# Performance work log

Hardware: AMD Instinct MI355X
Metric: run time of the kernel (lower is better)

The kernel has to match this reference:

```python
import math
import jax, jax.numpy as jnp
import numpy as np

B, T_ALL, D = 128, 197, 768
T = T_ALL - 1
ORG, E, DFF, NCLS = 5, 8, 1024, 100
CAP_FACTOR = 1.25
MAX_K = 2  # training=True -> min(2, n_experts)


def setup_inputs() -> dict:
    key = jax.random.key(0)
    ks = jax.random.split(key, 16)
    s = lambda *sh: 0.02
    inp = {
        "tokens": jax.random.normal(ks[0], (B, T_ALL, D), jnp.float32),
        "organ_priors": jax.random.uniform(ks[1], (B, ORG), jnp.float32),
        "router_w": jax.random.normal(ks[2], (D + ORG, E), jnp.float32) * 0.02,
        "router_b": jnp.zeros((E,), jnp.float32),
        "w1": jax.random.normal(ks[3], (E, D, DFF), jnp.float32) * 0.02,
        "b1": jnp.zeros((E, DFF), jnp.float32),
        "w2": jax.random.normal(ks[4], (E, DFF, D), jnp.float32) * 0.02,
        "b2": jnp.zeros((E, D), jnp.float32),
        "ln_g": jnp.ones((D,), jnp.float32),
        "ln_b": jnp.zeros((D,), jnp.float32),
        "cls_w": jax.random.normal(ks[5], (D, NCLS), jnp.float32) * 0.02,
        "cls_b": jnp.zeros((NCLS,), jnp.float32),
        "aux_w": jax.random.normal(ks[6], (D, ORG), jnp.float32) * 0.02,
        "aux_b": jnp.zeros((ORG,), jnp.float32),
    }
    return inp


def switch_moe(flat, flat_prior, router_w, router_b, w1, b1, w2, b2):
    N = flat.shape[0]
    capacity = math.ceil(N / E * CAP_FACTOR)  # static
    logits = jnp.concatenate([flat, flat_prior], axis=-1) @ router_w + router_b  # (N,E)
    probs = jax.nn.softmax(logits, axis=-1)
    entropy = -(probs * jnp.log(probs + 1e-12)).sum(-1)  # (N,)
    topk_vals, topk_idx = jax.lax.top_k(probs, MAX_K)  # (N,K)
    topk_probs = topk_vals / (topk_vals.sum(-1, keepdims=True) + 1e-12)
    # one-hot expert assignment over top-k slots: (N,E)
    sel = jnp.any(topk_idx[:, None, :] == jnp.arange(E)[None, :, None], axis=-1)
    # combine weight per (token, expert): first (unique) matching top-k slot's prob
    w_full = (topk_probs[:, None, :] * (topk_idx[:, None, :] == jnp.arange(E)[None, :, None])).sum(-1)  # (N,E)
    # capacity-limited dispatch: per expert keep top-`capacity` tokens by router prob
    score = jnp.where(sel, probs, -jnp.inf).T  # (E,N)
    top_scores, idx = jax.lax.top_k(score, capacity)  # (E,cap), sorted desc like torch.sort
    valid = jnp.isfinite(top_scores)  # (E,cap)
    gathered = flat[idx]  # (E,cap,D)
    h = jax.nn.gelu(jnp.einsum('ecd,edf->ecf', gathered, w1) + b1[:, None, :], approximate=False)
    out_sel = jnp.einsum('ecf,efd->ecd', h, w2) + b2[:, None, :]  # (E,cap,D)
    w_sel = jnp.take_along_axis(w_full.T, idx, axis=1) * valid  # (E,cap)
    flat_idx = idx.reshape(-1)
    outputs = jnp.zeros_like(flat).at[flat_idx].add((out_sel * w_sel[..., None]).reshape(-1, D))
    processed = jnp.zeros((N,), jnp.float32).at[flat_idx].add(valid.reshape(-1).astype(jnp.float32)) > 0
    outputs = jnp.where(processed[:, None], outputs, flat)
    return outputs, probs, entropy


def reference(tokens, organ_priors, router_w, router_b, w1, b1, w2, b2,
              ln_g, ln_b, cls_w, cls_b, aux_w, aux_b):
    cls = tokens[:, 0, :]                # (B,D)
    patches = tokens[:, 1:, :]           # (B,T,D)
    flat = patches.reshape(B * T, D)
    flat_prior = jnp.broadcast_to(organ_priors[:, None, :], (B, T, ORG)).reshape(B * T, ORG)
    out_flat, probs, entropy = switch_moe(flat, flat_prior, router_w, router_b, w1, b1, w2, b2)
    # cls token passes through MoE untouched (only patches go through switch)
    mu = cls.mean(-1, keepdims=True)
    var = ((cls - mu) ** 2).mean(-1, keepdims=True)
    cls_final = (cls - mu) * jax.lax.rsqrt(var + 1e-5) * ln_g + ln_b
    logits = cls_final @ cls_w + cls_b
    aux_org = cls_final @ aux_w + aux_b
    return logits, aux_org, probs.reshape(B, T, E), entropy.reshape(B, T)
```

## Files before the change

kernel.cpp:

```cpp
#include <hip/hip_runtime.h>
#include <hip/hip_bf16.h>
#include <math.h>

#define NB     128
#define NT_ALL 197
#define NT     196
#define ND     768
#define NORG   5
#define NE     8
#define NCLS   100
#define NCOL   105
#define NTOK   (NB * NT)
#define KB     24
#define PF     6

#define CBLKS  256
#define RBLKS  392

typedef short  bf16x8 __attribute__((ext_vector_type(8)));
typedef float  f32x4  __attribute__((ext_vector_type(4)));


__global__ __launch_bounds__(256, 4) void fused_kernel(
    const float* __restrict__ tokens,
    const float* __restrict__ priors,
    const float* __restrict__ rw,
    const float* __restrict__ rbias,
    const float* __restrict__ ln_g, const float* __restrict__ ln_b,
    const float* __restrict__ cls_w,
    const float* __restrict__ cls_b,
    const float* __restrict__ aux_w,
    const float* __restrict__ aux_b,
    float* __restrict__ out_logits,
    float* __restrict__ out_aux,
    float* __restrict__ probs_out,
    float* __restrict__ ent_out)
{
    const int t = threadIdx.x;

    if (blockIdx.x >= CBLKS) {
        const int rblk = blockIdx.x - CBLKS;

        __shared__ __align__(16) __hip_bfloat16 s_a[KB * 4 * 16 * 8];
        __shared__ float s_pl[2][NE];

        const int wid  = t >> 6;
        const int lane = t & 63;
        const int tok0 = rblk * 64;
        const int gbase = tok0 + wid * 16;
        const int tt = lane & 15;
        const int g  = lane >> 4;
        const int token = gbase + tt;
        const int b  = token / NT;
        const float* xp = tokens + ((size_t)b * NT_ALL + 1 + (token - b * NT)) * ND
                          + g * 8;

        float4 xb[PF][2];
#pragma unroll
        for (int i = 0; i < PF; ++i) {
            xb[i][0] = *reinterpret_cast<const float4*>(xp + i * 32);
            xb[i][1] = *reinterpret_cast<const float4*>(xp + i * 32 + 4);
        }

        {
            bf16x8 z = {0, 0, 0, 0, 0, 0, 0, 0};
            bf16x8* p = (bf16x8*)s_a;
            for (int i = t; i < KB * 4 * 8; i += 256)
                p[(i >> 3) * 16 + 8 + (i & 7)] = z;
        }
        for (int i = t; i < ND * NE; i += 256) {
            const int k = i >> 3, e = i & 7;
            const int kb = k >> 5, gg = (k >> 3) & 3, j = k & 7;
            s_a[(((kb * 4 + gg) * 16) + e) * 8 + j] = __float2bfloat16(rw[i]);
        }
        const int b0 = tok0 / NT;
        const int b1 = (tok0 + 63) / NT;
        if (t < 16) {
            const int e = t & 7, which = t >> 3;
            const int bb = which ? b1 : b0;
            float a = rbias[e];
#pragma unroll
            for (int o = 0; o < NORG; ++o)
                a = fmaf(priors[bb * NORG + o], rw[(ND + o) * NE + e], a);
            s_pl[which][e] = a;
        }
        __syncthreads();

        const bf16x8* s_a8 = (const bf16x8*)s_a;
        f32x4 acc0 = {0.f, 0.f, 0.f, 0.f};
        f32x4 acc1 = {0.f, 0.f, 0.f, 0.f};

#pragma unroll
        for (int kb = 0; kb < KB; ++kb) {
            const float4 x0 = xb[kb % PF][0];
            const float4 x1 = xb[kb % PF][1];
            union { bf16x8 v; __hip_bfloat16 h[8]; } u;
            u.h[0] = __float2bfloat16(x0.x);
            u.h[1] = __float2bfloat16(x0.y);
            u.h[2] = __float2bfloat16(x0.z);
            u.h[3] = __float2bfloat16(x0.w);
            u.h[4] = __float2bfloat16(x1.x);
            u.h[5] = __float2bfloat16(x1.y);
            u.h[6] = __float2bfloat16(x1.z);
            u.h[7] = __float2bfloat16(x1.w);
            const bf16x8 af = s_a8[(kb * 4 + g) * 16 + tt];
            if (kb & 1)
                acc1 = __builtin_amdgcn_mfma_f32_16x16x32_bf16(af, u.v, acc1, 0, 0, 0);
            else
                acc0 = __builtin_amdgcn_mfma_f32_16x16x32_bf16(af, u.v, acc0, 0, 0, 0);
            if (kb + PF < KB) {
                xb[kb % PF][0] = *reinterpret_cast<const float4*>(xp + (kb + PF) * 32);
                xb[kb % PF][1] = *reinterpret_cast<const float4*>(xp + (kb + PF) * 32 + 4);
            }
        }
        const f32x4 acc = acc0 + acc1;

        const float p0 = __shfl_xor(acc[0], 16, 64);
        const float p1 = __shfl_xor(acc[1], 16, 64);
        const float p2 = __shfl_xor(acc[2], 16, 64);
        const float p3 = __shfl_xor(acc[3], 16, 64);

        if (lane < 16) {
            float lg[NE] = {acc[0], acc[1], acc[2], acc[3], p0, p1, p2, p3};
            const int bsel = (token >= (b0 + 1) * NT) ? 1 : 0;
#pragma unroll
            for (int e = 0; e < NE; ++e) lg[e] += s_pl[bsel][e];

            float m = lg[0];
#pragma unroll
            for (int e = 1; e < NE; ++e) m = fmaxf(m, lg[e]);
            float S = 0.f, dd = 0.f;
#pragma unroll
            for (int e = 0; e < NE; ++e) {
                const float l = lg[e] - m;
                const float p = __expf(l);
                lg[e] = p;
                S += p;
                dd = fmaf(p, l, dd);
            }
            const float inv = 1.f / S;
            const float ent = __logf(S) - dd * inv;

            float4 q0 = {lg[0] * inv, lg[1] * inv, lg[2] * inv, lg[3] * inv};
            float4 q1 = {lg[4] * inv, lg[5] * inv, lg[6] * inv, lg[7] * inv};
            *reinterpret_cast<float4*>(probs_out + (size_t)token * NE)     = q0;
            *reinterpret_cast<float4*>(probs_out + (size_t)token * NE + 4) = q1;
            ent_out[token] = ent;
        }
    } else {
        const int cb   = blockIdx.x;
        const int b    = cb >> 1;
        const int half = cb & 1;
        const int lane = t & 63;
        const int wv   = t >> 6;

        __shared__ __align__(16) float s_x[ND];
        __shared__ float s_red[4];
        __shared__ float s_part[4][65];

        const float* xp = tokens + (size_t)b * NT_ALL * ND;

        float sum = 0.f;
        for (int i = t; i < ND; i += 256) { float v = xp[i]; s_x[i] = v; sum += v; }
#pragma unroll
        for (int off = 32; off; off >>= 1) sum += __shfl_xor(sum, off, 64);
        if (lane == 0) s_red[wv] = sum;
        __syncthreads();
        const float mu = (s_red[0] + s_red[1] + s_red[2] + s_red[3]) * (1.f / ND);
        __syncthreads();

        float sq = 0.f;
        for (int i = t; i < ND; i += 256) { float d = s_x[i] - mu; sq += d * d; }
#pragma unroll
        for (int off = 32; off; off >>= 1) sq += __shfl_xor(sq, off, 64);
        if (lane == 0) s_red[wv] = sq;
        __syncthreads();
        const float var  = (s_red[0] + s_red[1] + s_red[2] + s_red[3]) * (1.f / ND);
        const float rstd = rsqrtf(var + 1e-5f);
        __syncthreads();

        for (int i = t; i < ND; i += 256)
            s_x[i] = (s_x[i] - mu) * rstd * ln_g[i] + ln_b[i];
        __syncthreads();

        const int c = half * 64 + lane;
        const float* wp; int st;
        if (c < NCLS)      { wp = cls_w + c;          st = NCLS; }
        else if (c < NCOL) { wp = aux_w + (c - NCLS); st = NORG; }
        else               { wp = aux_w;              st = NORG; }

        const int d0 = wv * 192;
        const float* w = wp + (size_t)d0 * st;
        const int st2 = 2 * st, st3 = 3 * st, st4 = 4 * st;
        float a0 = 0.f, a1 = 0.f, a2 = 0.f, a3 = 0.f;
#pragma unroll 8
        for (int j = 0; j < 192; j += 4) {
            const float4 x4 = *reinterpret_cast<const float4*>(&s_x[d0 + j]);
            a0 = fmaf(x4.x, w[0],   a0);
            a1 = fmaf(x4.y, w[st],  a1);
            a2 = fmaf(x4.z, w[st2], a2);
            a3 = fmaf(x4.w, w[st3], a3);
            w += st4;
        }
        s_part[wv][lane] = (a0 + a1) + (a2 + a3);
        __syncthreads();

        if (t < 64) {
            float r = s_part[0][t] + s_part[1][t] + s_part[2][t] + s_part[3][t];
            const int cc = half * 64 + t;
            if (cc < NCLS)
                out_logits[b * NCLS + cc] = r + cls_b[cc];
            else if (cc < NCOL)
                out_aux[b * NORG + (cc - NCLS)] = r + aux_b[cc - NCLS];
        }
    }
}

extern "C" void kernel_launch(void* const* d_in, const int* in_sizes, int n_in,
                              void* d_out, int out_size, void* d_ws, size_t ws_size,
                              hipStream_t stream) {
    const float* tokens = (const float*)d_in[0];
    const float* priors = (const float*)d_in[1];
    const float* rw     = (const float*)d_in[2];
    const float* rbias  = (const float*)d_in[3];
    const float* ln_g   = (const float*)d_in[8];
    const float* ln_b   = (const float*)d_in[9];
    const float* cls_w  = (const float*)d_in[10];
    const float* cls_b  = (const float*)d_in[11];
    const float* aux_w  = (const float*)d_in[12];
    const float* aux_b  = (const float*)d_in[13];

    float* out = (float*)d_out;
    float* out_logits = out;
    float* out_aux    = out + NB * NCLS;
    float* out_probs  = out + NB * NCLS + NB * NORG;
    float* out_ent    = out + NB * NCLS + NB * NORG + (size_t)NTOK * NE;

    fused_kernel<<<CBLKS + RBLKS, 256, 0, stream>>>(
        tokens, priors, rw, rbias, ln_g, ln_b, cls_w, cls_b, aux_w, aux_b,
        out_logits, out_aux, out_probs, out_ent);
}
```

Baseline: 25.96 us.

## Precompute bf16 router weight fragments in a prepass and read them from global memory

A separate prepass kernel converts the router weights into MFMA-ready bf16 fragments and computes the per-batch prior+bias logit offsets, writing both to workspace. Each router block then skips its per-block LDS staging, conversion and __syncthreads, and instead loads the A fragments directly from global (L2-cached), prefetched one step ahead. Router blocks are also moved to the front of the grid ahead of the classifier blocks. The cost is an extra kernel launch and a dependency between the two kernels.

```diff
diff --git a/kernel.cpp b/kernel.cpp
--- a/kernel.cpp
+++ b/kernel.cpp
@@ -14,18 +14,54 @@
 #define KB     24
 #define PF     6
 
+#define RBLKS  392
 #define CBLKS  256
-#define RBLKS  392
+
+#define NFRAG  (KB * 64)
+#define WS_A_BYTES  (NFRAG * 16)
+#define WS_PL_OFF   WS_A_BYTES
 
 typedef short  bf16x8 __attribute__((ext_vector_type(8)));
 typedef float  f32x4  __attribute__((ext_vector_type(4)));
 
 
+__global__ __launch_bounds__(256) void prepass_kernel(
+    const float* __restrict__ rw,
+    const float* __restrict__ rbias,
+    const float* __restrict__ priors,
+    __hip_bfloat16* __restrict__ ws_a,
+    float* __restrict__ ws_pl)
+{
+    const int gi = blockIdx.x * 256 + threadIdx.x;
+    if (gi < NFRAG) {
+        const int e  = gi & 15;
+        const int kg = gi >> 4;
+        union { bf16x8 v; __hip_bfloat16 h[8]; } u;
+        if (e < 8) {
+#pragma unroll
+            for (int j = 0; j < 8; ++j)
+                u.h[j] = __float2bfloat16(rw[(kg * 8 + j) * NE + e]);
+        } else {
+#pragma unroll
+            for (int j = 0; j < 8; ++j)
+                u.h[j] = __float2bfloat16(0.f);
+        }
+        reinterpret_cast<bf16x8*>(ws_a)[gi] = u.v;
+    } else if (gi < NFRAG + NB * NE) {
+        const int i = gi - NFRAG;
+        const int b = i >> 3, e = i & 7;
+        float a = rbias[e];
+#pragma unroll
+        for (int o = 0; o < NORG; ++o)
+            a = fmaf(priors[b * NORG + o], rw[(ND + o) * NE + e], a);
+        ws_pl[i] = a;
+    }
+}
+
 __global__ __launch_bounds__(256, 4) void fused_kernel(
     const float* __restrict__ tokens,
-    const float* __restrict__ priors,
-    const float* __restrict__ rw,
-    const float* __restrict__ rbias,
+    const __hip_bfloat16* __restrict__ ws_a,
+    const float* __restrict__ ws_pl,
     const float* __restrict__ ln_g, const float* __restrict__ ln_b,
     const float* __restrict__ cls_w,
     const float* __restrict__ cls_b,
@@ -38,22 +74,16 @@
 {
     const int t = threadIdx.x;
 
-    if (blockIdx.x >= CBLKS) {
-        const int rblk = blockIdx.x - CBLKS;
-
-        __shared__ __align__(16) __hip_bfloat16 s_a[KB * 4 * 16 * 8];
-        __shared__ float s_pl[2][NE];
-
+    if (blockIdx.x < RBLKS) {
         const int wid  = t >> 6;
         const int lane = t & 63;
-        const int tok0 = rblk * 64;
-        const int gbase = tok0 + wid * 16;
-        const int tt = lane & 15;
-        const int g  = lane >> 4;
-        const int token = gbase + tt;
+        const int tt   = lane & 15;
+        const int g    = lane >> 4;
+        const int token = (blockIdx.x * 4 + wid) * 16 + tt;
         const int b  = token / NT;
         const float* xp = tokens + ((size_t)b * NT_ALL + 1 + (token - b * NT)) * ND
                           + g * 8;
+        const bf16x8* afp = reinterpret_cast<const bf16x8*>(ws_a) + lane;
 
         float4 xb[PF][2];
 #pragma unroll
@@ -61,37 +91,14 @@
             xb[i][0] = *reinterpret_cast<const float4*>(xp + i * 32);
             xb[i][1] = *reinterpret_cast<const float4*>(xp + i * 32 + 4);
         }
-
-        {
-            bf16x8 z = {0, 0, 0, 0, 0, 0, 0, 0};
-            bf16x8* p = (bf16x8*)s_a;
-            for (int i = t; i < KB * 4 * 8; i += 256)
-                p[(i >> 3) * 16 + 8 + (i & 7)] = z;
-        }
-        for (int i = t; i < ND * NE; i += 256) {
-            const int k = i >> 3, e = i & 7;
-            const int kb = k >> 5, gg = (k >> 3) & 3, j = k & 7;
-            s_a[(((kb * 4 + gg) * 16) + e) * 8 + j] = __float2bfloat16(rw[i]);
-        }
-        const int b0 = tok0 / NT;
-        const int b1 = (tok0 + 63) / NT;
-        if (t < 16) {
-            const int e = t & 7, which = t >> 3;
-            const int bb = which ? b1 : b0;
-            float a = rbias[e];
-#pragma unroll
-            for (int o = 0; o < NORG; ++o)
-                a = fmaf(priors[bb * NORG + o], rw[(ND + o) * NE + e], a);
-            s_pl[which][e] = a;
-        }
-        __syncthreads();
-
-        const bf16x8* s_a8 = (const bf16x8*)s_a;
+        bf16x8 af_cur = afp[0];
+
         f32x4 acc0 = {0.f, 0.f, 0.f, 0.f};
         f32x4 acc1 = {0.f, 0.f, 0.f, 0.f};
 
 #pragma unroll
         for (int kb = 0; kb < KB; ++kb) {
+            const bf16x8 af_next = (kb + 1 < KB) ? afp[(kb + 1) * 64] : af_cur;
             const float4 x0 = xb[kb % PF][0];
             const float4 x1 = xb[kb % PF][1];
             union { bf16x8 v; __hip_bfloat16 h[8]; } u;
@@ -103,15 +110,15 @@
             u.h[5] = __float2bfloat16(x1.y);
             u.h[6] = __float2bfloat16(x1.z);
             u.h[7] = __float2bfloat16(x1.w);
-            const bf16x8 af = s_a8[(kb * 4 + g) * 16 + tt];
             if (kb & 1)
-                acc1 = __builtin_amdgcn_mfma_f32_16x16x32_bf16(af, u.v, acc1, 0, 0, 0);
+                acc1 = __builtin_amdgcn_mfma_f32_16x16x32_bf16(af_cur, u.v, acc1, 0, 0, 0);
             else
-                acc0 = __builtin_amdgcn_mfma_f32_16x16x32_bf16(af, u.v, acc0, 0, 0, 0);
+                acc0 = __builtin_amdgcn_mfma_f32_16x16x32_bf16(af_cur, u.v, acc0, 0, 0, 0);
             if (kb + PF < KB) {
                 xb[kb % PF][0] = *reinterpret_cast<const float4*>(xp + (kb + PF) * 32);
                 xb[kb % PF][1] = *reinterpret_cast<const float4*>(xp + (kb + PF) * 32 + 4);
             }
+            af_cur = af_next;
         }
         const f32x4 acc = acc0 + acc1;
 
@@ -122,9 +129,10 @@
 
         if (lane < 16) {
             float lg[NE] = {acc[0], acc[1], acc[2], acc[3], p0, p1, p2, p3};
-            const int bsel = (token >= (b0 + 1) * NT) ? 1 : 0;
-#pragma unroll
-            for (int e = 0; e < NE; ++e) lg[e] += s_pl[bsel][e];
+            const float4 pl0 = *reinterpret_cast<const float4*>(ws_pl + b * NE);
+            const float4 pl1 = *reinterpret_cast<const float4*>(ws_pl + b * NE + 4);
+            lg[0] += pl0.x; lg[1] += pl0.y; lg[2] += pl0.z; lg[3] += pl0.w;
+            lg[4] += pl1.x; lg[5] += pl1.y; lg[6] += pl1.z; lg[7] += pl1.w;
 
             float m = lg[0];
 #pragma unroll
@@ -148,7 +156,7 @@
             ent_out[token] = ent;
         }
     } else {
-        const int cb   = blockIdx.x;
+        const int cb   = blockIdx.x - RBLKS;
         const int b    = cb >> 1;
         const int half = cb & 1;
         const int lane = t & 63;
@@ -236,7 +244,14 @@
     float* out_probs  = out + NB * NCLS + NB * NORG;
     float* out_ent    = out + NB * NCLS + NB * NORG + (size_t)NTOK * NE;
 
-    fused_kernel<<<CBLKS + RBLKS, 256, 0, stream>>>(
-        tokens, priors, rw, rbias, ln_g, ln_b, cls_w, cls_b, aux_w, aux_b,
+    __hip_bfloat16* ws_a = (__hip_bfloat16*)d_ws;
+    float*          ws_pl = (float*)((char*)d_ws + WS_PL_OFF);
+
+    const int pre_items = NFRAG + NB * NE;
+    prepass_kernel<<<(pre_items + 255) / 256, 256, 0, stream>>>(
+        rw, rbias, priors, ws_a, ws_pl);
+
+    fused_kernel<<<RBLKS + CBLKS, 256, 0, stream>>>(
+        tokens, ws_a, ws_pl, ln_g, ln_b, cls_w, cls_b, aux_w, aux_b,
         out_logits, out_aux, out_probs, out_ent);
 }
```

Result: slower. 30.22 us (+16.4%).

## Split router K-reduction across wave pairs and double router block count

Applied to the files above, without the earlier changes.

Each router block now covers 32 tokens instead of 64, and two waves split the 768-wide K dimension per 16-token group, combining their partial MFMA accumulators through shared memory. Router blocks are also placed ahead of the classifier blocks in the grid. The goal is more parallelism and shorter per-wave dependency chains for a bandwidth-bound token read. The cost is that the bf16 router weights are converted into LDS twice as often, and each block gains an extra barrier and shared-memory reduction.

```diff
diff --git a/kernel.cpp b/kernel.cpp
--- a/kernel.cpp
+++ b/kernel.cpp
@@ -12,10 +12,11 @@
 #define NCOL   105
 #define NTOK   (NB * NT)
 #define KB     24
+#define KHALF  12
 #define PF     6
 
+#define RBLKS  784
 #define CBLKS  256
-#define RBLKS  392
 
 typedef short  bf16x8 __attribute__((ext_vector_type(8)));
 typedef float  f32x4  __attribute__((ext_vector_type(4)));
@@ -38,22 +39,22 @@
 {
     const int t = threadIdx.x;
 
-    if (blockIdx.x >= CBLKS) {
-        const int rblk = blockIdx.x - CBLKS;
-
+    if (blockIdx.x < RBLKS) {
         __shared__ __align__(16) __hip_bfloat16 s_a[KB * 4 * 16 * 8];
         __shared__ float s_pl[2][NE];
+        __shared__ __align__(16) float s_acc[2][64][4];
 
         const int wid  = t >> 6;
         const int lane = t & 63;
-        const int tok0 = rblk * 64;
-        const int gbase = tok0 + wid * 16;
-        const int tt = lane & 15;
-        const int g  = lane >> 4;
-        const int token = gbase + tt;
+        const int pair = wid >> 1;
+        const int half = wid & 1;
+        const int tt   = lane & 15;
+        const int g    = lane >> 4;
+        const int tok0 = blockIdx.x * 32;
+        const int token = tok0 + pair * 16 + tt;
         const int b  = token / NT;
         const float* xp = tokens + ((size_t)b * NT_ALL + 1 + (token - b * NT)) * ND
-                          + g * 8;
+                          + half * (KHALF * 32) + g * 8;
 
         float4 xb[PF][2];
 #pragma unroll
@@ -74,7 +75,7 @@
             s_a[(((kb * 4 + gg) * 16) + e) * 8 + j] = __float2bfloat16(rw[i]);
         }
         const int b0 = tok0 / NT;
-        const int b1 = (tok0 + 63) / NT;
+        const int b1 = (tok0 + 31) / NT;
         if (t < 16) {
             const int e = t & 7, which = t >> 3;
             const int bb = which ? b1 : b0;
@@ -86,12 +87,12 @@
         }
         __syncthreads();
 
-        const bf16x8* s_a8 = (const bf16x8*)s_a;
+        const bf16x8* s_a8 = (const bf16x8*)s_a + (half * KHALF * 4 + g) * 16 + tt;
         f32x4 acc0 = {0.f, 0.f, 0.f, 0.f};
         f32x4 acc1 = {0.f, 0.f, 0.f, 0.f};
 
 #pragma unroll
-        for (int kb = 0; kb < KB; ++kb) {
+        for (int kb = 0; kb < KHALF; ++kb) {
             const float4 x0 = xb[kb % PF][0];
             const float4 x1 = xb[kb % PF][1];
             union { bf16x8 v; __hip_bfloat16 h[8]; } u;
@@ -103,52 +104,60 @@
             u.h[5] = __float2bfloat16(x1.y);
             u.h[6] = __float2bfloat16(x1.z);
             u.h[7] = __float2bfloat16(x1.w);
-            const bf16x8 af = s_a8[(kb * 4 + g) * 16 + tt];
+            const bf16x8 af = s_a8[kb * 64];
             if (kb & 1)
                 acc1 = __builtin_amdgcn_mfma_f32_16x16x32_bf16(af, u.v, acc1, 0, 0, 0);
             else
                 acc0 = __builtin_amdgcn_mfma_f32_16x16x32_bf16(af, u.v, acc0, 0, 0, 0);
-            if (kb + PF < KB) {
+            if (kb + PF < KHALF) {
                 xb[kb % PF][0] = *reinterpret_cast<const float4*>(xp + (kb + PF) * 32);
                 xb[kb % PF][1] = *reinterpret_cast<const float4*>(xp + (kb + PF) * 32 + 4);
             }
         }
-        const f32x4 acc = acc0 + acc1;
-
-        const float p0 = __shfl_xor(acc[0], 16, 64);
-        const float p1 = __shfl_xor(acc[1], 16, 64);
-        const float p2 = __shfl_xor(acc[2], 16, 64);
-        const float p3 = __shfl_xor(acc[3], 16, 64);
-
-        if (lane < 16) {
-            float lg[NE] = {acc[0], acc[1], acc[2], acc[3], p0, p1, p2, p3};
-            const int bsel = (token >= (b0 + 1) * NT) ? 1 : 0;
-#pragma unroll
-            for (int e = 0; e < NE; ++e) lg[e] += s_pl[bsel][e];
-
-            float m = lg[0];
-#pragma unroll
-            for (int e = 1; e < NE; ++e) m = fmaxf(m, lg[e]);
-            float S = 0.f, dd = 0.f;
-#pragma unroll
-            for (int e = 0; e < NE; ++e) {
-                const float l = lg[e] - m;
-                const float p = __expf(l);
-                lg[e] = p;
-                S += p;
-                dd = fmaf(p, l, dd);
+        f32x4 acc = acc0 + acc1;
+
+        if (half == 1)
+            *reinterpret_cast<f32x4*>(&s_acc[pair][lane][0]) = acc;
+        __syncthreads();
+
+        if (half == 0) {
+            acc += *reinterpret_cast<const f32x4*>(&s_acc[pair][lane][0]);
+
+            const float p0 = __shfl_xor(acc[0], 16, 64);
+            const float p1 = __shfl_xor(acc[1], 16, 64);
+            const float p2 = __shfl_xor(acc[2], 16, 64);
+            const float p3 = __shfl_xor(acc[3], 16, 64);
+
+            if (lane < 16) {
+                float lg[NE] = {acc[0], acc[1], acc[2], acc[3], p0, p1, p2, p3};
+                const int bsel = (b == b0) ? 0 : 1;
+#pragma unroll
+                for (int e = 0; e < NE; ++e) lg[e] += s_pl[bsel][e];
+
+                float m = lg[0];
+#pragma unroll
+                for (int e = 1; e < NE; ++e) m = fmaxf(m, lg[e]);
+                float S = 0.f, dd = 0.f;
+#pragma unroll
+                for (int e = 0; e < NE; ++e) {
+                    const float l = lg[e] - m;
+                    const float p = __expf(l);
+                    lg[e] = p;
+                    S += p;
+                    dd = fmaf(p, l, dd);
+                }
+                const float inv = 1.f / S;
+                const float ent = __logf(S) - dd * inv;
+
+                float4 q0 = {lg[0] * inv, lg[1] * inv, lg[2] * inv, lg[3] * inv};
+                float4 q1 = {lg[4] * inv, lg[5] * inv, lg[6] * inv, lg[7] * inv};
+                *reinterpret_cast<float4*>(probs_out + (size_t)token * NE)     = q0;
+                *reinterpret_cast<float4*>(probs_out + (size_t)token * NE + 4) = q1;
+                ent_out[token] = ent;
             }
-            const float inv = 1.f / S;
-            const float ent = __logf(S) - dd * inv;
-
-            float4 q0 = {lg[0] * inv, lg[1] * inv, lg[2] * inv, lg[3] * inv};
-            float4 q1 = {lg[4] * inv, lg[5] * inv, lg[6] * inv, lg[7] * inv};
-            *reinterpret_cast<float4*>(probs_out + (size_t)token * NE)     = q0;
-            *reinterpret_cast<float4*>(probs_out + (size_t)token * NE + 4) = q1;
-            ent_out[token] = ent;
         }
     } else {
-        const int cb   = blockIdx.x;
+        const int cb   = blockIdx.x - RBLKS;
         const int b    = cb >> 1;
         const int half = cb & 1;
         const int lane = t & 63;
@@ -236,7 +245,7 @@
     float* out_probs  = out + NB * NCLS + NB * NORG;
     float* out_ent    = out + NB * NCLS + NB * NORG + (size_t)NTOK * NE;
 
-    fused_kernel<<<CBLKS + RBLKS, 256, 0, stream>>>(
+    fused_kernel<<<RBLKS + CBLKS, 256, 0, stream>>>(
         tokens, priors, rw, rbias, ln_g, ln_b, cls_w, cls_b, aux_w, aux_b,
         out_logits, out_aux, out_probs, out_ent);
 }
```

After: 29.60 us. 1.14x slower.
